# Kernel tuning notes

Measured on AMD Instinct MI355X. Metric: run time of the kernel, lower is better.

Reference implementation:

```python
import jax, jax.numpy as jnp
import numpy as np

WIN = 1022       # window_length == frame_length == fft_length
HOP = 256        # hop_length
SIG_LEN = 33216  # signal_length
FACTOR = 2       # downsampling factor
T_IN = 127       # input STFT frames
B = 64
L_OLA = (T_IN - 1) * HOP + WIN  # 33278, length produced by inverse_stft

# indices kept after the strided deletion (evens < SIG_LEN, plus OLA tail beyond SIG_LEN)
KEEP = np.concatenate([np.arange(0, SIG_LEN, FACTOR), np.arange(SIG_LEN, L_OLA)])
L_OUT = KEEP.shape[0]                # 16670
T_OUT = 1 + (L_OUT - WIN) // HOP     # 62 output STFT frames

def _hann(n):
    # periodic Hann, matches tf.signal.hann_window default
    return (0.5 - 0.5 * np.cos(2.0 * np.pi * np.arange(n) / n)).astype(np.float32)

def _synth_window():
    # tf.signal.inverse_stft_window_fn(HOP): w / overlap-added w^2 (periodic form)
    w = _hann(WIN)
    d = w * w
    overlaps = -(-WIN // HOP)
    d = np.pad(d, (0, overlaps * HOP - WIN))
    d = d.reshape(-1, HOP).sum(0)      # per-phase sum of squares
    d = np.tile(d, overlaps)[:WIN]
    return (w / d).astype(np.float32)

WINDOW = jnp.asarray(_hann(WIN))
SYNTH = jnp.asarray(_synth_window())
OLA_IDX = jnp.asarray((np.arange(T_IN)[:, None] * HOP + np.arange(WIN)[None, :]).reshape(-1))
FRAME_IDX = jnp.asarray(np.arange(T_OUT)[:, None] * HOP + np.arange(WIN)[None, :])
KEEP_J = jnp.asarray(KEEP)

def setup_inputs() -> dict:
    key = jax.random.key(0)
    return {"inputs": jax.random.normal(key, (B, 512, T_IN, 2), dtype=jnp.float32)}

def reference(inputs):
    # inputs: [B, 512, T, 2] (real/imag stacked STFT)
    stfts = jax.lax.complex(inputs[..., 0], inputs[..., 1])   # [B, 512, T]
    stfts = jnp.transpose(stfts, (0, 2, 1))                   # [B, T, 512]
    # inverse_stft: irfft per frame, apply synthesis window, overlap-add
    frames = jnp.fft.irfft(stfts, n=WIN, axis=-1) * SYNTH
    b = frames.shape[0]
    sig = jnp.zeros((b, L_OLA), frames.dtype).at[:, OLA_IDX].add(frames.reshape(b, -1))
    # strided index deletion (the unstack/del/stack loop) == single gather
    sig = sig[:, KEEP_J]                                      # [B, 16670]
    # forward STFT
    fr = sig[:, FRAME_IDX] * WINDOW
    S = jnp.fft.rfft(fr, n=WIN, axis=-1)                      # [B, T_OUT, 512]
    S = jnp.transpose(S, (0, 2, 1))                           # [B, 512, T_OUT]
    return jnp.stack([jnp.real(S), jnp.imag(S)], axis=-1)     # [B, 512, T_OUT, 2]
```

## Files before the change

kernel.cpp:

```cpp
#include <hip/hip_runtime.h>


#define WIN       1022
#define HOP       256
#define T_IN      127
#define NB        64
#define NPAD      1024
#define L_OLA     33278
#define L_OUT     16670
#define T_OUT     62
#define HALF_KEPT 16608
#define ROWS1     (NB * T_IN)
#define ROWS1P    8192
#define ROWS2     (NB * T_OUT)
#define ROWS2P    4096
#define TWO_PI_F  6.28318530717958647692f

typedef _Float16 half8 __attribute__((ext_vector_type(8)));
typedef float    f32x4 __attribute__((ext_vector_type(4)));


__global__ void build_windows(float* __restrict__ synth, float* __restrict__ window) {
    int j = blockIdx.x * blockDim.x + threadIdx.x;
    if (j >= NPAD) return;
    if (j >= WIN) { synth[j] = 0.f; window[j] = 0.f; return; }
    const float c = TWO_PI_F / (float)WIN;
    float w = 0.5f - 0.5f * cosf(c * (float)j);
    int p = j & (HOP - 1);
    float dd = 0.f;
    for (int r = 0; r < 4; ++r) {
        int idx = p + HOP * r;
        if (idx < WIN) {
            float wi = 0.5f - 0.5f * cosf(c * (float)idx);
            dd += wi * wi;
        }
    }
    synth[j]  = w / dd;
    window[j] = w;
}

__global__ void build_m1t(_Float16* __restrict__ M1T, const float* __restrict__ synth) {
    int idx = blockIdx.x * blockDim.x + threadIdx.x;
    int j = idx >> 10, kk = idx & 1023;
    float v = 0.f;
    if (j < WIN) {
        int k = kk >> 1, c = kk & 1;
        if (!(c == 1 && (k == 0 || k == 511))) {
            float a = (k == 0 || k == 511) ? (1.f / (float)WIN) : (2.f / (float)WIN);
            int m = (k * j) % WIN;
            float ang = (float)m * (TWO_PI_F / (float)WIN);
            float s, co;
            __sincosf(ang, &s, &co);
            v = a * synth[j] * (c == 0 ? co : -s);
        }
    }
    M1T[idx] = (_Float16)v;
}

__global__ void build_m2t(_Float16* __restrict__ M2T, const float* __restrict__ window) {
    int idx = blockIdx.x * blockDim.x + threadIdx.x;
    int col = idx >> 10, j = idx & 1023;
    float v = 0.f;
    if (j < WIN) {
        int k = col >> 1, c = col & 1;
        int m = (k * j) % WIN;
        float ang = (float)m * (TWO_PI_F / (float)WIN);
        float s, co;
        __sincosf(ang, &s, &co);
        v = window[j] * (c == 0 ? co : -s);
    }
    M2T[idx] = (_Float16)v;
}

__global__ __launch_bounds__(256) void pack_a(const float* __restrict__ in,
                                              _Float16* __restrict__ A1) {
    __shared__ float lds[32 * 254];
    int tid = threadIdx.x;
    int k0 = blockIdx.x * 32;
    int b  = blockIdx.y;
    if (b == NB) {
        for (int f = tid; f < 64 * 64; f += 256) {
            int r = f >> 6, cc = f & 63;
            A1[(size_t)(ROWS1 + r) * NPAD + 2 * k0 + cc] = (_Float16)0.f;
        }
        return;
    }
    const float* base = in + ((size_t)b * 512 + k0) * (T_IN * 2);
    for (int idx = tid; idx < 32 * 254; idx += 256)
        lds[idx] = base[idx];
    __syncthreads();
    for (int f = tid; f < T_IN * 64; f += 256) {
        int t = f >> 6, l = f & 63;
        int dk = l >> 1, c = l & 1;
        A1[(size_t)(b * T_IN + t) * NPAD + 2 * k0 + l] =
            (_Float16)lds[dk * 254 + t * 2 + c];
    }
}


__device__ __forceinline__ void stage16(const void* g, void* l) {
    __builtin_amdgcn_global_load_lds(
        (const __attribute__((address_space(1))) unsigned int*)g,
        (__attribute__((address_space(3))) unsigned int*)l, 16, 0, 0);
}

__device__ __forceinline__ void stage_tile(const _Float16* __restrict__ G,
                                           int row0, int k0,
                                           _Float16* __restrict__ L, int tid) {
    int r = tid >> 2, ko = (tid & 3) * 8;
    stage16(G + (size_t)(row0 + r) * NPAD + k0 + ko,       L + r * 32 + ko);
    stage16(G + (size_t)(row0 + 64 + r) * NPAD + k0 + ko,  L + (64 + r) * 32 + ko);
}

template <bool IS_GEMM2>
__global__ __launch_bounds__(256) void gemm_mfma(const _Float16* __restrict__ A,
                                                 const _Float16* __restrict__ Bt,
                                                 void* __restrict__ Cv) {
    __shared__ __align__(16) _Float16 As[128 * 32];
    __shared__ __align__(16) _Float16 Bs[128 * 32];

    int tid  = threadIdx.x;
    int lane = tid & 63, wave = tid >> 6;
    int quad = lane >> 4, l16 = lane & 15;
    int rowOff = (wave >> 1) * 64, colOff = (wave & 1) * 64;
    int rowBase = blockIdx.y * 128, colBase = blockIdx.x * 128;

    f32x4 acc[4][4] = {};

    for (int k0 = 0; k0 < NPAD; k0 += 32) {
        stage_tile(A,  rowBase, k0, As, tid);
        stage_tile(Bt, colBase, k0, Bs, tid);
        __syncthreads();

        half8 af[4], bf[4];
#pragma unroll
        for (int i = 0; i < 4; ++i)
            af[i] = *(const half8*)&As[(rowOff + i * 16 + l16) * 32 + quad * 8];
#pragma unroll
        for (int j = 0; j < 4; ++j)
            bf[j] = *(const half8*)&Bs[(colOff + j * 16 + l16) * 32 + quad * 8];
#pragma unroll
        for (int i = 0; i < 4; ++i)
#pragma unroll
            for (int j = 0; j < 4; ++j)
                acc[i][j] = __builtin_amdgcn_mfma_f32_16x16x32_f16(af[i], bf[j], acc[i][j], 0, 0, 0);
        __syncthreads();
    }

#pragma unroll
    for (int i = 0; i < 4; ++i) {
#pragma unroll
        for (int j = 0; j < 4; ++j) {
            int col = colBase + colOff + j * 16 + l16;
#pragma unroll
            for (int r = 0; r < 4; ++r) {
                int row = rowBase + rowOff + i * 16 + quad * 4 + r;
                if (!IS_GEMM2) {
                    ((_Float16*)Cv)[(size_t)row * NPAD + col] = (_Float16)acc[i][j][r];
                } else if (row < ROWS2) {
                    int b = row / T_OUT, t2 = row % T_OUT;
                    int k = col >> 1, c = col & 1;
                    ((float*)Cv)[(((size_t)b * 512 + k) * T_OUT + t2) * 2 + c] = acc[i][j][r];
                }
            }
        }
    }
}

__global__ void ola_pack(const _Float16* __restrict__ frames,
                         _Float16* __restrict__ fr) {
    int i = blockIdx.x * 256 + threadIdx.x;
    int b = blockIdx.y;
    if (i >= L_OUT) return;
    int s = (i < HALF_KEPT) ? (2 * i) : (i + HALF_KEPT);

    int tmin = (s > WIN - 1) ? ((s - (WIN - 1) + HOP - 1) >> 8) : 0;
    int tmax = s >> 8; if (tmax > T_IN - 1) tmax = T_IN - 1;
    float v = 0.f;
    for (int t = tmin; t <= tmax; ++t)
        v += (float)frames[(size_t)(b * T_IN + t) * NPAD + (s - t * HOP)];

    _Float16 hv = (_Float16)v;
    int t2min = (i > WIN - HOP - 1) ? ((i - (WIN - 1) + HOP - 1) >> 8) : 0;
    int t2max = i >> 8; if (t2max > T_OUT - 1) t2max = T_OUT - 1;
    for (int t2 = t2min; t2 <= t2max; ++t2)
        fr[(size_t)(b * T_OUT + t2) * NPAD + (i - t2 * HOP)] = hv;
}


extern "C" void kernel_launch(void* const* d_in, const int* in_sizes, int n_in,
                              void* d_out, int out_size, void* d_ws, size_t ws_size,
                              hipStream_t stream) {
    const float* in = (const float*)d_in[0];
    float* out = (float*)d_out;
    char* ws = (char*)d_ws;

    _Float16* M1T    = (_Float16*)ws;
    _Float16* M2T    = M1T + (size_t)NPAD * NPAD;
    _Float16* A1     = M2T + (size_t)NPAD * NPAD;
    _Float16* fr     = A1 + (size_t)ROWS1P * NPAD;
    _Float16* frames = fr + (size_t)ROWS2P * NPAD;
    float*    synth  = (float*)(frames + (size_t)ROWS1P * NPAD);
    float*    window = synth + NPAD;

    build_windows<<<4, 256, 0, stream>>>(synth, window);
    build_m1t<<<(NPAD * NPAD) / 256, 256, 0, stream>>>(M1T, synth);
    build_m2t<<<(NPAD * NPAD) / 256, 256, 0, stream>>>(M2T, window);
    pack_a<<<dim3(16, NB + 1), 256, 0, stream>>>(in, A1);
    gemm_mfma<false><<<dim3(NPAD / 128, ROWS1P / 128), 256, 0, stream>>>(A1, M1T, frames);
    hipMemsetAsync(fr, 0, (size_t)ROWS2P * NPAD * sizeof(_Float16), stream);
    ola_pack<<<dim3((L_OUT + 255) / 256, NB), 256, 0, stream>>>(frames, fr);
    gemm_mfma<true><<<dim3(NPAD / 128, ROWS2P / 128), 256, 0, stream>>>(fr, M2T, out);
}
```

Measured before the change: 161.4 us.

## Compute only even-indexed iSTFT samples and fuse setup kernels into one prep launch

GEMM1 now produces only the even-position frame samples that survive the factor-2 decimation. It reads every other row of M1T through a doubled pitch, which halves the first GEMM's N dimension. The few odd tail samples are computed directly in ola_pack with per-thread dot products. The window, matrix-building and packing kernels are merged into one prep launch, the memset and zero-padding writes are dropped, and the GEMM tile shrinks to 128x64. This removes wasted FLOPs and launch overhead, at the cost of a slow serial dot-product path for the tail and reliance on padding regions being zero or ignored.

```diff
diff --git a/kernel.cpp b/kernel.cpp
--- a/kernel.cpp
+++ b/kernel.cpp
@@ -6,93 +6,79 @@
 #define T_IN      127
 #define NB        64
 #define NPAD      1024
-#define L_OLA     33278
-#define L_OUT     16670
+#define NE        512
 #define T_OUT     62
 #define HALF_KEPT 16608
-#define ROWS1     (NB * T_IN)
+#define L_USE     16638
+#define ROWS1     8128
 #define ROWS1P    8192
-#define ROWS2     (NB * T_OUT)
+#define ROWS2     3968
 #define ROWS2P    4096
 #define TWO_PI_F  6.28318530717958647692f
 
 typedef _Float16 half8 __attribute__((ext_vector_type(8)));
 typedef float    f32x4 __attribute__((ext_vector_type(4)));
 
-
-__global__ void build_windows(float* __restrict__ synth, float* __restrict__ window) {
-    int j = blockIdx.x * blockDim.x + threadIdx.x;
-    if (j >= NPAD) return;
-    if (j >= WIN) { synth[j] = 0.f; window[j] = 0.f; return; }
-    const float c = TWO_PI_F / (float)WIN;
-    float w = 0.5f - 0.5f * cosf(c * (float)j);
-    int p = j & (HOP - 1);
-    float dd = 0.f;
-    for (int r = 0; r < 4; ++r) {
-        int idx = p + HOP * r;
-        if (idx < WIN) {
-            float wi = 0.5f - 0.5f * cosf(c * (float)idx);
-            dd += wi * wi;
-        }
-    }
-    synth[j]  = w / dd;
-    window[j] = w;
-}
-
-__global__ void build_m1t(_Float16* __restrict__ M1T, const float* __restrict__ synth) {
-    int idx = blockIdx.x * blockDim.x + threadIdx.x;
-    int j = idx >> 10, kk = idx & 1023;
-    float v = 0.f;
-    if (j < WIN) {
-        int k = kk >> 1, c = kk & 1;
-        if (!(c == 1 && (k == 0 || k == 511))) {
-            float a = (k == 0 || k == 511) ? (1.f / (float)WIN) : (2.f / (float)WIN);
+__global__ __launch_bounds__(256) void prep(const float* __restrict__ in,
+                                            _Float16* __restrict__ M1T,
+                                            _Float16* __restrict__ M2T,
+                                            _Float16* __restrict__ A1) {
+    __shared__ float lds[32 * 254];
+    int bx = blockIdx.x, tid = threadIdx.x;
+    const float cc = TWO_PI_F / (float)WIN;
+
+    if (bx < 4096) {
+        int idx = bx * 256 + tid, j = idx >> 10, kk = idx & 1023;
+        if ((j & 1) && j < 961) return;
+        float v = 0.f;
+        if (j < WIN) {
+            float w = 0.5f - 0.5f * __cosf(cc * (float)j);
+            float dd = 0.f;
+            int p = j & (HOP - 1);
+            for (int r = 0; r < 4; ++r) {
+                int ix = p + HOP * r;
+                if (ix < WIN) {
+                    float wi = 0.5f - 0.5f * __cosf(cc * (float)ix);
+                    dd += wi * wi;
+                }
+            }
+            float synth = w / dd;
+            int k = kk >> 1, c = kk & 1;
+            if (!(c == 1 && (k == 0 || k == 511))) {
+                float a = (k == 0 || k == 511) ? (1.f / (float)WIN) : (2.f / (float)WIN);
+                int m = (k * j) % WIN;
+                float s, co;
+                __sincosf((float)m * cc, &s, &co);
+                v = a * synth * (c == 0 ? co : -s);
+            }
+        }
+        M1T[idx] = (_Float16)v;
+        return;
+    }
+    if (bx < 8192) {
+        int idx = (bx - 4096) * 256 + tid, col = idx >> 10, j = idx & 1023;
+        float v = 0.f;
+        if (j < WIN) {
+            float w = 0.5f - 0.5f * __cosf(cc * (float)j);
+            int k = col >> 1, c = col & 1;
             int m = (k * j) % WIN;
-            float ang = (float)m * (TWO_PI_F / (float)WIN);
             float s, co;
-            __sincosf(ang, &s, &co);
-            v = a * synth[j] * (c == 0 ? co : -s);
-        }
-    }
-    M1T[idx] = (_Float16)v;
-}
-
-__global__ void build_m2t(_Float16* __restrict__ M2T, const float* __restrict__ window) {
-    int idx = blockIdx.x * blockDim.x + threadIdx.x;
-    int col = idx >> 10, j = idx & 1023;
-    float v = 0.f;
-    if (j < WIN) {
-        int k = col >> 1, c = col & 1;
-        int m = (k * j) % WIN;
-        float ang = (float)m * (TWO_PI_F / (float)WIN);
-        float s, co;
-        __sincosf(ang, &s, &co);
-        v = window[j] * (c == 0 ? co : -s);
-    }
-    M2T[idx] = (_Float16)v;
-}
-
-__global__ __launch_bounds__(256) void pack_a(const float* __restrict__ in,
-                                              _Float16* __restrict__ A1) {
-    __shared__ float lds[32 * 254];
-    int tid = threadIdx.x;
-    int k0 = blockIdx.x * 32;
-    int b  = blockIdx.y;
-    if (b == NB) {
-        for (int f = tid; f < 64 * 64; f += 256) {
-            int r = f >> 6, cc = f & 63;
-            A1[(size_t)(ROWS1 + r) * NPAD + 2 * k0 + cc] = (_Float16)0.f;
-        }
+            __sincosf((float)m * cc, &s, &co);
+            v = w * (c == 0 ? co : -s);
+        }
+        M2T[idx] = (_Float16)v;
         return;
     }
-    const float* base = in + ((size_t)b * 512 + k0) * (T_IN * 2);
-    for (int idx = tid; idx < 32 * 254; idx += 256)
-        lds[idx] = base[idx];
+    int bx2 = bx - 8192;
+    int kt = bx2 >> 6, b = bx2 & 63;
+    const float* base = in + ((size_t)b * 512 + kt * 32) * (T_IN * 2);
+    for (int idx2 = tid; idx2 < 32 * 254; idx2 += 256)
+        lds[idx2] = base[idx2];
     __syncthreads();
     for (int f = tid; f < T_IN * 64; f += 256) {
         int t = f >> 6, l = f & 63;
         int dk = l >> 1, c = l & 1;
-        A1[(size_t)(b * T_IN + t) * NPAD + 2 * k0 + l] =
+        A1[(size_t)(b * T_IN + t) * NPAD + kt * 64 + l] =
             (_Float16)lds[dk * 254 + t * 2 + c];
     }
 }
@@ -104,45 +90,43 @@
         (__attribute__((address_space(3))) unsigned int*)l, 16, 0, 0);
 }
 
-__device__ __forceinline__ void stage_tile(const _Float16* __restrict__ G,
-                                           int row0, int k0,
-                                           _Float16* __restrict__ L, int tid) {
-    int r = tid >> 2, ko = (tid & 3) * 8;
-    stage16(G + (size_t)(row0 + r) * NPAD + k0 + ko,       L + r * 32 + ko);
-    stage16(G + (size_t)(row0 + 64 + r) * NPAD + k0 + ko,  L + (64 + r) * 32 + ko);
-}
-
-template <bool IS_GEMM2>
+template <bool G2, int BPITCH, int CPITCH>
 __global__ __launch_bounds__(256) void gemm_mfma(const _Float16* __restrict__ A,
-                                                 const _Float16* __restrict__ Bt,
+                                                 const _Float16* __restrict__ B0,
                                                  void* __restrict__ Cv) {
     __shared__ __align__(16) _Float16 As[128 * 32];
-    __shared__ __align__(16) _Float16 Bs[128 * 32];
+    __shared__ __align__(16) _Float16 Bs[64 * 32];
 
     int tid  = threadIdx.x;
     int lane = tid & 63, wave = tid >> 6;
     int quad = lane >> 4, l16 = lane & 15;
-    int rowOff = (wave >> 1) * 64, colOff = (wave & 1) * 64;
-    int rowBase = blockIdx.y * 128, colBase = blockIdx.x * 128;
-
-    f32x4 acc[4][4] = {};
+    int rowOff = (wave >> 1) * 64, colOff = (wave & 1) * 32;
+    int rowBase = blockIdx.y * 128, colBase = blockIdx.x * 64;
+
+    int r = tid >> 2, ko = (tid & 3) * 8;
+    const _Float16* Arow0 = A + (size_t)(rowBase + r) * NPAD + ko;
+    const _Float16* Arow1 = Arow0 + (size_t)64 * NPAD;
+    const _Float16* Brow  = B0 + (size_t)(colBase + r) * BPITCH + ko;
+
+    f32x4 acc[4][2] = {};
 
     for (int k0 = 0; k0 < NPAD; k0 += 32) {
-        stage_tile(A,  rowBase, k0, As, tid);
-        stage_tile(Bt, colBase, k0, Bs, tid);
+        stage16(Arow0 + k0, As + r * 32 + ko);
+        stage16(Arow1 + k0, As + (64 + r) * 32 + ko);
+        stage16(Brow  + k0, Bs + r * 32 + ko);
         __syncthreads();
 
-        half8 af[4], bf[4];
+        half8 af[4], bf[2];
 #pragma unroll
         for (int i = 0; i < 4; ++i)
             af[i] = *(const half8*)&As[(rowOff + i * 16 + l16) * 32 + quad * 8];
 #pragma unroll
-        for (int j = 0; j < 4; ++j)
+        for (int j = 0; j < 2; ++j)
             bf[j] = *(const half8*)&Bs[(colOff + j * 16 + l16) * 32 + quad * 8];
 #pragma unroll
         for (int i = 0; i < 4; ++i)
 #pragma unroll
-            for (int j = 0; j < 4; ++j)
+            for (int j = 0; j < 2; ++j)
                 acc[i][j] = __builtin_amdgcn_mfma_f32_16x16x32_f16(af[i], bf[j], acc[i][j], 0, 0, 0);
         __syncthreads();
     }
@@ -150,38 +134,59 @@
 #pragma unroll
     for (int i = 0; i < 4; ++i) {
 #pragma unroll
-        for (int j = 0; j < 4; ++j) {
+        for (int j = 0; j < 2; ++j) {
             int col = colBase + colOff + j * 16 + l16;
 #pragma unroll
-            for (int r = 0; r < 4; ++r) {
-                int row = rowBase + rowOff + i * 16 + quad * 4 + r;
-                if (!IS_GEMM2) {
-                    ((_Float16*)Cv)[(size_t)row * NPAD + col] = (_Float16)acc[i][j][r];
+            for (int rr = 0; rr < 4; ++rr) {
+                int row = rowBase + rowOff + i * 16 + quad * 4 + rr;
+                if (!G2) {
+                    ((_Float16*)Cv)[(size_t)row * CPITCH + col] = (_Float16)acc[i][j][rr];
                 } else if (row < ROWS2) {
                     int b = row / T_OUT, t2 = row % T_OUT;
                     int k = col >> 1, c = col & 1;
-                    ((float*)Cv)[(((size_t)b * 512 + k) * T_OUT + t2) * 2 + c] = acc[i][j][r];
+                    ((float*)Cv)[(((size_t)b * 512 + k) * T_OUT + t2) * 2 + c] = acc[i][j][rr];
                 }
             }
         }
     }
 }
 
-__global__ void ola_pack(const _Float16* __restrict__ frames,
+__global__ void ola_pack(const _Float16* __restrict__ fe,
+                         const _Float16* __restrict__ A1,
+                         const _Float16* __restrict__ M1T,
                          _Float16* __restrict__ fr) {
     int i = blockIdx.x * 256 + threadIdx.x;
     int b = blockIdx.y;
-    if (i >= L_OUT) return;
-    int s = (i < HALF_KEPT) ? (2 * i) : (i + HALF_KEPT);
-
-    int tmin = (s > WIN - 1) ? ((s - (WIN - 1) + HOP - 1) >> 8) : 0;
-    int tmax = s >> 8; if (tmax > T_IN - 1) tmax = T_IN - 1;
+    if (i >= L_USE) return;
+
     float v = 0.f;
-    for (int t = tmin; t <= tmax; ++t)
-        v += (float)frames[(size_t)(b * T_IN + t) * NPAD + (s - t * HOP)];
+    if (i < HALF_KEPT) {
+        int tmin = (i > 510) ? ((i - 383) >> 7) : 0;
+        int tmax = i >> 7; if (tmax > T_IN - 1) tmax = T_IN - 1;
+        for (int t = tmin; t <= tmax; ++t)
+            v += (float)fe[(size_t)(b * T_IN + t) * NE + (i - t * 128)];
+    } else {
+        int s = i + HALF_KEPT;
+        int p = s - 32256;
+        if (!(s & 1)) {
+            v = (float)fe[(size_t)(b * T_IN + 126) * NE + (p >> 1)];
+        } else {
+            const _Float16* ar = A1 + (size_t)(b * T_IN + 126) * NPAD;
+            const _Float16* mr = M1T + (size_t)p * NPAD;
+            float a0 = 0.f;
+            for (int k = 0; k < NPAD; k += 8) {
+                half8 av = *(const half8*)&ar[k];
+                half8 mv = *(const half8*)&mr[k];
+#pragma unroll
+                for (int u = 0; u < 8; ++u)
+                    a0 += (float)av[u] * (float)mv[u];
+            }
+            v = a0;
+        }
+    }
 
     _Float16 hv = (_Float16)v;
-    int t2min = (i > WIN - HOP - 1) ? ((i - (WIN - 1) + HOP - 1) >> 8) : 0;
+    int t2min = (i > WIN - 1) ? ((i - (WIN - 1) + HOP - 1) >> 8) : 0;
     int t2max = i >> 8; if (t2max > T_OUT - 1) t2max = T_OUT - 1;
     for (int t2 = t2min; t2 <= t2max; ++t2)
         fr[(size_t)(b * T_OUT + t2) * NPAD + (i - t2 * HOP)] = hv;
@@ -195,20 +200,14 @@
     float* out = (float*)d_out;
     char* ws = (char*)d_ws;
 
-    _Float16* M1T    = (_Float16*)ws;
-    _Float16* M2T    = M1T + (size_t)NPAD * NPAD;
-    _Float16* A1     = M2T + (size_t)NPAD * NPAD;
-    _Float16* fr     = A1 + (size_t)ROWS1P * NPAD;
-    _Float16* frames = fr + (size_t)ROWS2P * NPAD;
-    float*    synth  = (float*)(frames + (size_t)ROWS1P * NPAD);
-    float*    window = synth + NPAD;
-
-    build_windows<<<4, 256, 0, stream>>>(synth, window);
-    build_m1t<<<(NPAD * NPAD) / 256, 256, 0, stream>>>(M1T, synth);
-    build_m2t<<<(NPAD * NPAD) / 256, 256, 0, stream>>>(M2T, window);
-    pack_a<<<dim3(16, NB + 1), 256, 0, stream>>>(in, A1);
-    gemm_mfma<false><<<dim3(NPAD / 128, ROWS1P / 128), 256, 0, stream>>>(A1, M1T, frames);
-    hipMemsetAsync(fr, 0, (size_t)ROWS2P * NPAD * sizeof(_Float16), stream);
-    ola_pack<<<dim3((L_OUT + 255) / 256, NB), 256, 0, stream>>>(frames, fr);
-    gemm_mfma<true><<<dim3(NPAD / 128, ROWS2P / 128), 256, 0, stream>>>(fr, M2T, out);
-}
+    _Float16* M1T = (_Float16*)ws;
+    _Float16* M2T = M1T + (size_t)NPAD * NPAD;
+    _Float16* A1  = M2T + (size_t)NPAD * NPAD;
+    _Float16* fr  = A1 + (size_t)ROWS1P * NPAD;
+    _Float16* fe  = fr + (size_t)ROWS2P * NPAD;
+
+    prep<<<9216, 256, 0, stream>>>(in, M1T, M2T, A1);
+    gemm_mfma<false, 2 * NPAD, NE><<<dim3(NE / 64, ROWS1P / 128), 256, 0, stream>>>(A1, M1T, fe);
+    ola_pack<<<dim3(65, NB), 256, 0, stream>>>(fe, A1, M1T, fr);
+    gemm_mfma<true, NPAD, 0><<<dim3(NPAD / 64, ROWS2P / 128), 256, 0, stream>>>(fr, M2T, out);
+}
```

Result: faster. 156.5 us (-3.0%).
